# Performance work log

Hardware: AMD Instinct MI355X
Metric: run time of the kernel (lower is better)

## Reference

```python
import jax, jax.numpy as jnp
import numpy as np

EPS = 1e-12  # torch F.normalize eps


def setup_inputs() -> dict:
    key = jax.random.key(0)
    k1, k2, k3, k4, k5 = jax.random.split(key, 5)
    N, C, H, W = 32, 512, 32, 32
    E = 1024   # expansion * dim
    G = 8      # group
    D = E // G # 128, per-group channel dim
    K = 64     # num_clusters
    x = jax.random.normal(k1, (N, C, H, W), dtype=jnp.float32)
    W1 = jax.random.normal(k2, (E, C), dtype=jnp.float32) / np.sqrt(C)
    W2 = jax.random.normal(k3, (G, E), dtype=jnp.float32) / np.sqrt(E)
    Wc = jax.random.normal(k4, (K, D), dtype=jnp.float32) / np.sqrt(D)
    centroids = jax.random.uniform(k5, (K, D), dtype=jnp.float32)
    return {"x": x, "W1": W1, "W2": W2, "Wc": Wc, "centroids": centroids}


def reference(x, W1, W2, Wc, centroids):
    # x: [N, C, H, W]; W1: [E, C]; W2: [G, E]; Wc: [K, D]; centroids: [K, D]
    N, C, H, W = x.shape
    E = W1.shape[0]
    G = W2.shape[0]
    K, D = Wc.shape
    P = H * W
    # descriptor-wise L2 normalization over channel dim
    norm = jnp.linalg.norm(x, axis=1, keepdims=True)
    x = x / jnp.maximum(norm, EPS)
    # linear1 on channels: [N, E, P]
    xe = jnp.einsum('ncp,ec->nep', x.reshape(N, C, P), W1)
    # grouped features: [N, G, D, P]
    xg = xe.reshape(N, G, D, P)
    # attention gate: sigmoid(linear2)  -> [N, G, P]
    att = jax.nn.sigmoid(jnp.einsum('nep,ge->ngp', xe, W2))
    # 1x1 conv = per-pixel matmul with cluster weights -> [N, G, K, P]
    soft_assign = jax.nn.softmax(jnp.einsum('ngdp,kd->ngkp', xg, Wc), axis=2)
    # combined per-(cluster,pixel) weight
    w = soft_assign * att[:, :, None, :]  # [N, G, K, P]
    # NetVLAD residual aggregation, algebraically decomposed to avoid the
    # giant [N,G,K,D,P] intermediate:
    #   vlad[n,k,d] = sum_{g,p} w * xg  -  centroids[k,d] * sum_{g,p} w
    agg = jnp.einsum('ngkp,ngdp->nkd', w, xg)  # [N, K, D]
    wsum = w.sum(axis=(1, 3))                  # [N, K]
    vlad = agg - wsum[:, :, None] * centroids[None]  # [N, K, D]
    return vlad.reshape(N, K * D)
```

## Files before the change

kernel.cpp:

```cpp
#include <hip/hip_runtime.h>


#define N_  32
#define C_  512
#define P_  1024
#define E_  1024
#define G_  8
#define D_  128
#define K_  64

typedef __attribute__((ext_vector_type(8))) short bf16x8;
typedef __attribute__((ext_vector_type(4))) float f32x4;

__device__ __forceinline__ unsigned short f2b(float f) {
    union { float f; unsigned u; } v; v.f = f;
    unsigned r = (v.u + 0x7FFFu + ((v.u >> 16) & 1u)) >> 16;
    return (unsigned short)r;
}
__device__ __forceinline__ float b2f(unsigned short h) {
    union { unsigned u; float f; } v; v.u = ((unsigned)h) << 16;
    return v.f;
}

__device__ __forceinline__ void gl_lds16(const void* g, void* l) {
    __builtin_amdgcn_global_load_lds(
        (const __attribute__((address_space(1))) void*)g,
        (__attribute__((address_space(3))) void*)l, 16, 0, 0);
}

#define SB  __builtin_amdgcn_sched_barrier(0)
#define BAR __builtin_amdgcn_s_barrier()
#define WAITV(n_) asm volatile("s_waitcnt vmcnt(" #n_ ")" ::: "memory")

__global__ __launch_bounds__(256) void k0_prep(const float* __restrict__ W1,
                                               const float* __restrict__ Wc,
                                               const float* __restrict__ W2,
                                               unsigned short* __restrict__ W1b,
                                               unsigned short* __restrict__ Vb,
                                               unsigned short* __restrict__ Wa) {
    int bid = blockIdx.x;
    int t = threadIdx.x;
    if (bid < 1024) {
        int i0 = bid * 512 + t;
        W1b[i0]       = f2b(W1[i0]);
        W1b[i0 + 256] = f2b(W1[i0 + 256]);
        int ch = bid & 1, k = (bid >> 1) & 63, g = bid >> 7;
        int c = ch * 256 + t;
        float acc = 0.f;
        #pragma unroll 8
        for (int d = 0; d < 128; ++d)
            acc += Wc[k * 128 + d] * W1[(g * 128 + d) * C_ + c];
        Vb[(g * 64 + k) * C_ + c] = f2b(acc);
    } else {
        __shared__ float red[256];
        int idx = bid - 1024;
        int g  = idx >> 4;
        int c0 = (idx & 15) * 32;
        int c  = c0 + (t & 31);
        int ec = t >> 5;
        float acc = 0.f;
        #pragma unroll 8
        for (int i = 0; i < 128; ++i) {
            int e = ec * 128 + i;
            acc += W2[g * E_ + e] * W1[e * C_ + c];
        }
        red[t] = acc;
        __syncthreads();
        if (t < 32) {
            float s = 0.f;
            #pragma unroll
            for (int j = 0; j < 8; ++j) s += red[j * 32 + t];
            Wa[g * C_ + c0 + t] = f2b(s);
        }
    }
}

__global__ __launch_bounds__(256) void k1_norm_att(const float* __restrict__ x,
                                                   const unsigned short* __restrict__ Wa,
                                                   unsigned short* __restrict__ xhat_t,
                                                   float* __restrict__ att_s) {
    __shared__ short xc[128 * 256];
    __shared__ short waL[8 * 512];
    __shared__ float attP[2 * 64 * 8];
    __shared__ float red[256];
    int n = blockIdx.y;
    int p0 = blockIdx.x * 64;
    int t = threadIdx.x;
    int ps = t & 63, cs = t >> 6;

    #pragma unroll
    for (int i = 0; i < 2; ++i) {
        int ch = i * 256 + t;
        *(bf16x8*)&waL[ch * 8] = *(const bf16x8*)&Wa[ch * 8];
    }

    float ss = 0.f;
    for (int i = 0; i < 128; ++i) {
        float v = x[((size_t)(n * C_ + cs * 128 + i)) * P_ + p0 + ps];
        ss += v * v;
        xc[i * 256 + t] = (short)f2b(v);
    }
    red[t] = ss;
    __syncthreads();
    if (t < 64) {
        float s = red[t] + red[64 + t] + red[128 + t] + red[192 + t];
        red[t] = 1.0f / fmaxf(sqrtf(s), 1e-12f);
    }
    __syncthreads();

    float r = red[ps];
    float accA[8];
    #pragma unroll
    for (int g = 0; g < 8; ++g) accA[g] = 0.f;

    size_t base = ((size_t)(n * P_ + p0 + ps)) * C_ + cs * 128;
    #pragma unroll
    for (int jj = 0; jj < 16; ++jj) {
        bf16x8 o;
        float xv[8];
        #pragma unroll
        for (int j = 0; j < 8; ++j) {
            xv[j] = b2f((unsigned short)xc[(jj * 8 + j) * 256 + t]) * r;
            o[j] = (short)f2b(xv[j]);
        }
        *(bf16x8*)&xhat_t[base + jj * 8] = o;
        #pragma unroll
        for (int g = 0; g < 8; ++g) {
            bf16x8 wa = *(const bf16x8*)&waL[g * 512 + cs * 128 + jj * 8];
            #pragma unroll
            for (int j = 0; j < 8; ++j)
                accA[g] += b2f((unsigned short)wa[j]) * xv[j];
        }
    }

    if (cs & 1) {
        #pragma unroll
        for (int g = 0; g < 8; ++g)
            attP[((cs >> 1) * 64 + ps) * 8 + g] = accA[g];
    }
    __syncthreads();
    if (!(cs & 1)) {
        #pragma unroll
        for (int g = 0; g < 8; ++g)
            attP[((cs >> 1) * 64 + ps) * 8 + g] += accA[g];
    }
    __syncthreads();
    if (cs == 0) {
        #pragma unroll
        for (int g = 0; g < 8; ++g) {
            float s = attP[(0 * 64 + ps) * 8 + g] + attP[(1 * 64 + ps) * 8 + g];
            att_s[((size_t)(n * G_ + g)) * P_ + p0 + ps] = 1.0f / (1.0f + __expf(-s));
        }
    }
}

__global__ __launch_bounds__(256) void k2_gemm_xe(const unsigned short* __restrict__ W1b,
                                                  const unsigned short* __restrict__ xhat_t,
                                                  unsigned short* __restrict__ xe) {
    __shared__ __align__(16) short As[128 * 64];
    __shared__ __align__(16) short Bs[128 * 64];
    int n = blockIdx.y;
    int e0 = (blockIdx.x >> 3) * 128;
    int p0 = (blockIdx.x & 7) * 128;
    int t = threadIdx.x;
    int w = t >> 6, l = t & 63, q = l >> 4, l15 = l & 15;
    int wr = w >> 1, wc = w & 1;

    f32x4 acc[4][4];
    #pragma unroll
    for (int mi = 0; mi < 4; ++mi)
        #pragma unroll
        for (int ni = 0; ni < 4; ++ni)
            acc[mi][ni] = (f32x4){0.f, 0.f, 0.f, 0.f};

    for (int ks = 0; ks < 8; ++ks) {
        int k0 = ks * 64;
        #pragma unroll
        for (int i = 0; i < 4; ++i) {
            int ch = i * 256 + t;
            int row = ch >> 3, c8 = ch & 7;
            gl_lds16(&W1b[(e0 + row) * C_ + k0 + ((c8 ^ (row & 7)) * 8)], &As[ch * 8]);
        }
        #pragma unroll
        for (int i = 0; i < 4; ++i) {
            int ch = i * 256 + t;
            int row = ch >> 3, c8 = ch & 7;
            gl_lds16(&xhat_t[((size_t)(n * P_ + p0 + row)) * C_ + k0 + ((c8 ^ (row & 7)) * 8)], &Bs[ch * 8]);
        }
        __syncthreads();

        #pragma unroll
        for (int kk = 0; kk < 2; ++kk) {
            bf16x8 af[4], bf[4];
            #pragma unroll
            for (int mi = 0; mi < 4; ++mi)
                af[mi] = *(const bf16x8*)&As[(wr * 64 + mi * 16 + l15) * 64 + (((kk * 4 + q) ^ (l15 & 7)) * 8)];
            #pragma unroll
            for (int ni = 0; ni < 4; ++ni)
                bf[ni] = *(const bf16x8*)&Bs[(wc * 64 + ni * 16 + l15) * 64 + (((kk * 4 + q) ^ (l15 & 7)) * 8)];
            #pragma unroll
            for (int mi = 0; mi < 4; ++mi)
                #pragma unroll
                for (int ni = 0; ni < 4; ++ni)
                    acc[mi][ni] = __builtin_amdgcn_mfma_f32_16x16x32_bf16(af[mi], bf[ni], acc[mi][ni], 0, 0, 0);
        }
        __syncthreads();
    }

    #pragma unroll
    for (int mi = 0; mi < 4; ++mi) {
        #pragma unroll
        for (int ni = 0; ni < 4; ++ni) {
            #pragma unroll
            for (int r = 0; r < 4; ++r) {
                int e = e0 + wr * 64 + mi * 16 + q * 4 + r;
                int p = p0 + wc * 64 + ni * 16 + l15;
                xe[((size_t)(n * E_ + e)) * P_ + p] = f2b(acc[mi][ni][r]);
            }
        }
    }
}

__device__ __forceinline__ void stage_s(short* sb, const unsigned short* __restrict__ Vb,
                                        const unsigned short* __restrict__ xhat_t,
                                        int g, int n, int p0c, int k0, int t) {
    {
        int row = t >> 3, c8 = t & 7;
        gl_lds16(&Vb[(g * 64 + row) * C_ + k0 + ((c8 ^ (row & 7)) * 8)], &sb[t * 8]);
    }
    #pragma unroll
    for (int i = 0; i < 2; ++i) {
        int ch = i * 512 + t;
        int row = ch >> 3, c8 = ch & 7;
        gl_lds16(&xhat_t[((size_t)(n * P_ + p0c + row)) * C_ + k0 + ((c8 ^ (row & 7)) * 8)],
                 &sb[4096 + ch * 8]);
    }
}

__device__ __forceinline__ void stage_xg(short* xglds, const unsigned short* __restrict__ xe,
                                         int n, int g, int p0c, int t) {
    #pragma unroll
    for (int i = 0; i < 4; ++i) {
        int ch = i * 512 + t;
        int row = ch >> 4, c16 = ch & 15;
        gl_lds16(&xe[((size_t)(n * E_ + g * 128 + row)) * P_ + p0c + ((c16 ^ (row & 7)) * 8)],
                 &xglds[ch * 8]);
    }
}

__device__ __forceinline__ void mfma_s(f32x4 acc[4], const short* sb, int w, int q, int l15) {
    #pragma unroll
    for (int kk = 0; kk < 2; ++kk) {
        bf16x8 af[4], bfr;
        #pragma unroll
        for (int mi = 0; mi < 4; ++mi)
            af[mi] = *(const bf16x8*)&sb[(mi * 16 + l15) * 64 + (((kk * 4 + q) ^ (l15 & 7)) * 8)];
        bfr = *(const bf16x8*)&sb[4096 + (w * 16 + l15) * 64 + (((kk * 4 + q) ^ (l15 & 7)) * 8)];
        #pragma unroll
        for (int mi = 0; mi < 4; ++mi)
            acc[mi] = __builtin_amdgcn_mfma_f32_16x16x32_bf16(af[mi], bfr, acc[mi], 0, 0, 0);
    }
}

__global__ __launch_bounds__(512, 4) void k4_assign_agg(const unsigned short* __restrict__ Vb,
                                                        const unsigned short* __restrict__ xhat_t,
                                                        const unsigned short* __restrict__ xe,
                                                        const float* __restrict__ att_s,
                                                        float* __restrict__ agg_part,
                                                        float* __restrict__ wsum_part) {
    __shared__ __align__(16) char smem[81920];
    short* S0    = (short*)smem;
    short* S1    = (short*)(smem + 24576);
    short* xglds = (short*)(smem + 49152);
    short* wlds  = (short*)smem;
    float* wred  = (float*)smem;

    int b = blockIdx.y * 16 + blockIdx.x;
    int work = (b & 7) * 64 + (b >> 3);
    int n = work >> 4, g = work & 7, ph = (work >> 3) & 1;

    int t = threadIdx.x;
    int w = t >> 6, l = t & 63, q = l >> 4, l15 = l & 15;
    int kh = w >> 2, dq = w & 3;

    f32x4 acc_a[2][2];
    #pragma unroll
    for (int mi = 0; mi < 2; ++mi)
        #pragma unroll
        for (int ni = 0; ni < 2; ++ni)
            acc_a[mi][ni] = (f32x4){0.f, 0.f, 0.f, 0.f};
    float wsp[16];
    #pragma unroll
    for (int j = 0; j < 16; ++j) wsp[j] = 0.f;

#define RND(CUR, NXT, KN) \
    stage_s(NXT, Vb, xhat_t, g, n, p0c, (KN) * 64, t); \
    WAITV(3); BAR; SB; \
    mfma_s(acc_s, CUR, w, q, l15); \
    BAR; SB;

    #pragma unroll 1
    for (int cc = 0; cc < 4; ++cc) {
        int p0c = ph * 512 + cc * 128;

        float av = att_s[(((size_t)(n * G_ + g)) * P_) + p0c + w * 16 + l15];

        f32x4 acc_s[4];
        #pragma unroll
        for (int mi = 0; mi < 4; ++mi)
            acc_s[mi] = (f32x4){0.f, 0.f, 0.f, 0.f};

        stage_s(S0, Vb, xhat_t, g, n, p0c, 0, t);
        RND(S0, S1, 1)
        RND(S1, S0, 2)
        RND(S0, S1, 3)
        RND(S1, S0, 4)
        RND(S0, S1, 5)
        RND(S1, S0, 6)
        stage_s(S1, Vb, xhat_t, g, n, p0c, 448, t);
        stage_xg(xglds, xe, n, g, p0c, t);
        WAITV(7); BAR; SB;
        mfma_s(acc_s, S0, w, q, l15);
        BAR; SB;
        WAITV(4); BAR; SB;
        mfma_s(acc_s, S1, w, q, l15);
        BAR; SB;

        {
            float m = -1e30f;
            #pragma unroll
            for (int mi = 0; mi < 4; ++mi)
                #pragma unroll
                for (int r = 0; r < 4; ++r)
                    m = fmaxf(m, acc_s[mi][r]);
            m = fmaxf(m, __shfl_xor(m, 16));
            m = fmaxf(m, __shfl_xor(m, 32));
            float s = 0.f;
            #pragma unroll
            for (int mi = 0; mi < 4; ++mi)
                #pragma unroll
                for (int r = 0; r < 4; ++r) {
                    float e = __expf(acc_s[mi][r] - m);
                    acc_s[mi][r] = e;
                    s += e;
                }
            s += __shfl_xor(s, 16);
            s += __shfl_xor(s, 32);

            float scale = av / s;

            #pragma unroll
            for (int mi = 0; mi < 4; ++mi)
                #pragma unroll
                for (int r = 0; r < 4; ++r) {
                    float wv = acc_s[mi][r] * scale;
                    wsp[mi * 4 + r] += wv;
                    wlds[(mi * 16 + q * 4 + r) * 136 + (w * 16 + l15)] = (short)f2b(wv);
                }
        }
        __syncthreads();

        #pragma unroll
        for (int pk = 0; pk < 4; ++pk) {
            bf16x8 a2[2], b2[2];
            #pragma unroll
            for (int mi = 0; mi < 2; ++mi)
                a2[mi] = *(const bf16x8*)&wlds[(kh * 32 + mi * 16 + l15) * 136 + pk * 32 + q * 8];
            #pragma unroll
            for (int ni = 0; ni < 2; ++ni)
                b2[ni] = *(const bf16x8*)&xglds[(dq * 32 + ni * 16 + l15) * 128
                                                + (((pk * 4 + q) ^ (l15 & 7)) * 8)];
            #pragma unroll
            for (int mi = 0; mi < 2; ++mi)
                #pragma unroll
                for (int ni = 0; ni < 2; ++ni)
                    acc_a[mi][ni] = __builtin_amdgcn_mfma_f32_16x16x32_bf16(a2[mi], b2[ni], acc_a[mi][ni], 0, 0, 0);
        }
        __syncthreads();
    }

    size_t base = (((size_t)(n * G_ + g)) * 2 + ph) * 64;
    #pragma unroll
    for (int mi = 0; mi < 2; ++mi)
        #pragma unroll
        for (int ni = 0; ni < 2; ++ni)
            #pragma unroll
            for (int r = 0; r < 4; ++r) {
                int k = kh * 32 + mi * 16 + q * 4 + r;
                int d = dq * 32 + ni * 16 + l15;
                agg_part[(base + k) * 128 + d] = acc_a[mi][ni][r];
            }

    #pragma unroll
    for (int j = 0; j < 16; ++j) {
        float v = wsp[j];
        v += __shfl_xor(v, 1);
        v += __shfl_xor(v, 2);
        v += __shfl_xor(v, 4);
        v += __shfl_xor(v, 8);
        if (l15 == 0) {
            int k = (j >> 2) * 16 + q * 4 + (j & 3);
            wred[w * 64 + k] = v;
        }
    }
    __syncthreads();
    if (t < 64) {
        float s = 0.f;
        #pragma unroll
        for (int wv = 0; wv < 8; ++wv)
            s += wred[wv * 64 + t];
        wsum_part[(((size_t)(n * G_ + g)) * 2 + ph) * 64 + t] = s;
    }
}

__global__ __launch_bounds__(256) void k5_final(const float* __restrict__ agg_part,
                                                const float* __restrict__ wsum_part,
                                                const float* __restrict__ centroids,
                                                float* __restrict__ out) {
    int idx = blockIdx.x * 256 + threadIdx.x;
    int d = idx & 127;
    int k = (idx >> 7) & 63;
    int n = idx >> 13;
    float ws = 0.f;
    #pragma unroll
    for (int g = 0; g < 8; ++g)
        #pragma unroll
        for (int ph = 0; ph < 2; ++ph)
            ws += wsum_part[(((size_t)(n * G_ + g)) * 2 + ph) * 64 + k];
    float agg = 0.f;
    #pragma unroll
    for (int g = 0; g < 8; ++g)
        #pragma unroll
        for (int ph = 0; ph < 2; ++ph)
            agg += agg_part[(((((size_t)(n * G_ + g)) * 2 + ph) * 64) + k) * 128 + d];
    out[idx] = agg - ws * centroids[k * 128 + d];
}

extern "C" void kernel_launch(void* const* d_in, const int* in_sizes, int n_in,
                              void* d_out, int out_size, void* d_ws, size_t ws_size,
                              hipStream_t stream) {
    const float* x         = (const float*)d_in[0];
    const float* W1        = (const float*)d_in[1];
    const float* W2        = (const float*)d_in[2];
    const float* Wc        = (const float*)d_in[3];
    const float* centroids = (const float*)d_in[4];
    float* out = (float*)d_out;

    char* ws = (char*)d_ws;
    unsigned short* W1b      = (unsigned short*)(ws + 0);
    unsigned short* Vb       = (unsigned short*)(ws + 1048576);
    unsigned short* xhat_t   = (unsigned short*)(ws + 1572864);
    unsigned short* xe       = (unsigned short*)(ws + 35127296);
    float*          att_s    = (float*)(ws + 102236160);
    float*          agg_part = (float*)(ws + 103284736);
    float*          wsum_part= (float*)(ws + 120061952);
    unsigned short* Wa       = (unsigned short*)(ws + 120193024);

    hipLaunchKernelGGL(k0_prep,        dim3(1152), dim3(256), 0, stream, W1, Wc, W2, W1b, Vb, Wa);
    hipLaunchKernelGGL(k1_norm_att,    dim3(16, 32), dim3(256), 0, stream, x, Wa, xhat_t, att_s);
    hipLaunchKernelGGL(k2_gemm_xe,     dim3(64, 32), dim3(256), 0, stream, W1b, xhat_t, xe);
    hipLaunchKernelGGL(k4_assign_agg,  dim3(16, 32), dim3(512), 0, stream, Vb, xhat_t, xe,
                       att_s, agg_part, wsum_part);
    hipLaunchKernelGGL(k5_final,       dim3(1024), dim3(256), 0, stream,
                       agg_part, wsum_part, centroids, out);
}
```

Before: 212.3 us.

## Eliminate xe GEMM by reassociating aggregation through W1 in assign kernel

Drops the separate kernel that materialised xe = W1·xhat for every pixel and stops reading it back. The assign kernel now computes Y = w·xhat^T over the 512 input channels per group, staged from a new channel-major copy of xhat written by the norm kernel. It then multiplies Y by that group's W1 slice to form the aggregate. This removes a large bf16 intermediate write and read plus a full GEMM launch. In exchange the norm kernel does strided 2-byte scatter writes, the assign kernel holds many more accumulators (register pressure), and Y is rounded to bf16 before the second product.

```diff
diff --git a/kernel.cpp b/kernel.cpp
--- a/kernel.cpp
+++ b/kernel.cpp
@@ -78,6 +78,7 @@
 __global__ __launch_bounds__(256) void k1_norm_att(const float* __restrict__ x,
                                                    const unsigned short* __restrict__ Wa,
                                                    unsigned short* __restrict__ xhat_t,
+                                                   unsigned short* __restrict__ xhat_cp,
                                                    float* __restrict__ att_s) {
     __shared__ short xc[128 * 256];
     __shared__ short waL[8 * 512];
@@ -125,6 +126,11 @@
         }
         *(bf16x8*)&xhat_t[base + jj * 8] = o;
         #pragma unroll
+        for (int j = 0; j < 8; ++j) {
+            int c = cs * 128 + jj * 8 + j;
+            xhat_cp[((size_t)(n * C_ + c)) * P_ + p0 + ps] = (unsigned short)o[j];
+        }
+        #pragma unroll
         for (int g = 0; g < 8; ++g) {
             bf16x8 wa = *(const bf16x8*)&waL[g * 512 + cs * 128 + jj * 8];
             #pragma unroll
@@ -150,73 +156,6 @@
         for (int g = 0; g < 8; ++g) {
             float s = attP[(0 * 64 + ps) * 8 + g] + attP[(1 * 64 + ps) * 8 + g];
             att_s[((size_t)(n * G_ + g)) * P_ + p0 + ps] = 1.0f / (1.0f + __expf(-s));
-        }
-    }
-}
-
-__global__ __launch_bounds__(256) void k2_gemm_xe(const unsigned short* __restrict__ W1b,
-                                                  const unsigned short* __restrict__ xhat_t,
-                                                  unsigned short* __restrict__ xe) {
-    __shared__ __align__(16) short As[128 * 64];
-    __shared__ __align__(16) short Bs[128 * 64];
-    int n = blockIdx.y;
-    int e0 = (blockIdx.x >> 3) * 128;
-    int p0 = (blockIdx.x & 7) * 128;
-    int t = threadIdx.x;
-    int w = t >> 6, l = t & 63, q = l >> 4, l15 = l & 15;
-    int wr = w >> 1, wc = w & 1;
-
-    f32x4 acc[4][4];
-    #pragma unroll
-    for (int mi = 0; mi < 4; ++mi)
-        #pragma unroll
-        for (int ni = 0; ni < 4; ++ni)
-            acc[mi][ni] = (f32x4){0.f, 0.f, 0.f, 0.f};
-
-    for (int ks = 0; ks < 8; ++ks) {
-        int k0 = ks * 64;
-        #pragma unroll
-        for (int i = 0; i < 4; ++i) {
-            int ch = i * 256 + t;
-            int row = ch >> 3, c8 = ch & 7;
-            gl_lds16(&W1b[(e0 + row) * C_ + k0 + ((c8 ^ (row & 7)) * 8)], &As[ch * 8]);
-        }
-        #pragma unroll
-        for (int i = 0; i < 4; ++i) {
-            int ch = i * 256 + t;
-            int row = ch >> 3, c8 = ch & 7;
-            gl_lds16(&xhat_t[((size_t)(n * P_ + p0 + row)) * C_ + k0 + ((c8 ^ (row & 7)) * 8)], &Bs[ch * 8]);
-        }
-        __syncthreads();
-
-        #pragma unroll
-        for (int kk = 0; kk < 2; ++kk) {
-            bf16x8 af[4], bf[4];
-            #pragma unroll
-            for (int mi = 0; mi < 4; ++mi)
-                af[mi] = *(const bf16x8*)&As[(wr * 64 + mi * 16 + l15) * 64 + (((kk * 4 + q) ^ (l15 & 7)) * 8)];
-            #pragma unroll
-            for (int ni = 0; ni < 4; ++ni)
-                bf[ni] = *(const bf16x8*)&Bs[(wc * 64 + ni * 16 + l15) * 64 + (((kk * 4 + q) ^ (l15 & 7)) * 8)];
-            #pragma unroll
-            for (int mi = 0; mi < 4; ++mi)
-                #pragma unroll
-                for (int ni = 0; ni < 4; ++ni)
-                    acc[mi][ni] = __builtin_amdgcn_mfma_f32_16x16x32_bf16(af[mi], bf[ni], acc[mi][ni], 0, 0, 0);
-        }
-        __syncthreads();
-    }
-
-    #pragma unroll
-    for (int mi = 0; mi < 4; ++mi) {
-        #pragma unroll
-        for (int ni = 0; ni < 4; ++ni) {
-            #pragma unroll
-            for (int r = 0; r < 4; ++r) {
-                int e = e0 + wr * 64 + mi * 16 + q * 4 + r;
-                int p = p0 + wc * 64 + ni * 16 + l15;
-                xe[((size_t)(n * E_ + e)) * P_ + p] = f2b(acc[mi][ni][r]);
-            }
         }
     }
 }
@@ -237,14 +176,14 @@
     }
 }
 
-__device__ __forceinline__ void stage_xg(short* xglds, const unsigned short* __restrict__ xe,
-                                         int n, int g, int p0c, int t) {
-    #pragma unroll
-    for (int i = 0; i < 4; ++i) {
+__device__ __forceinline__ void stage_x(short* xb, const unsigned short* __restrict__ xhat_cp,
+                                        int n, int p0c, int c0, int t) {
+    #pragma unroll
+    for (int i = 0; i < 2; ++i) {
         int ch = i * 512 + t;
         int row = ch >> 4, c16 = ch & 15;
-        gl_lds16(&xe[((size_t)(n * E_ + g * 128 + row)) * P_ + p0c + ((c16 ^ (row & 7)) * 8)],
-                 &xglds[ch * 8]);
+        gl_lds16(&xhat_cp[((size_t)(n * C_ + c0 + row)) * P_ + p0c + ((c16 ^ (row & 7)) * 8)],
+                 &xb[ch * 8]);
     }
 }
 
@@ -262,18 +201,38 @@
     }
 }
 
+__device__ __forceinline__ void mfma_y(f32x4 Ysl[2], const short* wlds, const short* XB,
+                                       int kh, int dq, int q, int l15) {
+    #pragma unroll
+    for (int pk = 0; pk < 4; ++pk) {
+        bf16x8 a2[2], bx;
+        #pragma unroll
+        for (int mi = 0; mi < 2; ++mi)
+            a2[mi] = *(const bf16x8*)&wlds[(kh * 32 + mi * 16 + l15) * 136 + pk * 32 + q * 8];
+        bx = *(const bf16x8*)&XB[(dq * 16 + l15) * 128 + (((pk * 4 + q) ^ (l15 & 7)) * 8)];
+        #pragma unroll
+        for (int mi = 0; mi < 2; ++mi)
+            Ysl[mi] = __builtin_amdgcn_mfma_f32_16x16x32_bf16(a2[mi], bx, Ysl[mi], 0, 0, 0);
+    }
+}
+
 __global__ __launch_bounds__(512, 4) void k4_assign_agg(const unsigned short* __restrict__ Vb,
+                                                        const unsigned short* __restrict__ W1b,
                                                         const unsigned short* __restrict__ xhat_t,
-                                                        const unsigned short* __restrict__ xe,
+                                                        const unsigned short* __restrict__ xhat_cp,
                                                         const float* __restrict__ att_s,
                                                         float* __restrict__ agg_part,
                                                         float* __restrict__ wsum_part) {
     __shared__ __align__(16) char smem[81920];
-    short* S0    = (short*)smem;
-    short* S1    = (short*)(smem + 24576);
-    short* xglds = (short*)(smem + 49152);
-    short* wlds  = (short*)smem;
-    float* wred  = (float*)smem;
+    short* S0   = (short*)smem;
+    short* S1   = (short*)(smem + 24576);
+    short* X0   = (short*)smem;
+    short* X1   = (short*)(smem + 16384);
+    short* wlds = (short*)(smem + 49152);
+    short* Ylds = (short*)smem;
+    short* Wg   = (short*)(smem + 65536);
+    float* wred = (float*)smem;
+    float* wred2 = (float*)(smem + 65536);
 
     int b = blockIdx.y * 16 + blockIdx.x;
     int work = (b & 7) * 64 + (b >> 3);
@@ -283,12 +242,12 @@
     int w = t >> 6, l = t & 63, q = l >> 4, l15 = l & 15;
     int kh = w >> 2, dq = w & 3;
 
-    f32x4 acc_a[2][2];
-    #pragma unroll
-    for (int mi = 0; mi < 2; ++mi)
-        #pragma unroll
-        for (int ni = 0; ni < 2; ++ni)
-            acc_a[mi][ni] = (f32x4){0.f, 0.f, 0.f, 0.f};
+    f32x4 Y[8][2];
+    #pragma unroll
+    for (int sl = 0; sl < 8; ++sl)
+        #pragma unroll
+        for (int mi = 0; mi < 2; ++mi)
+            Y[sl][mi] = (f32x4){0.f, 0.f, 0.f, 0.f};
     float wsp[16];
     #pragma unroll
     for (int j = 0; j < 16; ++j) wsp[j] = 0.f;
@@ -297,6 +256,12 @@
     stage_s(NXT, Vb, xhat_t, g, n, p0c, (KN) * 64, t); \
     WAITV(3); BAR; SB; \
     mfma_s(acc_s, CUR, w, q, l15); \
+    BAR; SB;
+
+#define YRND(SL, CUR, NXT, CN) \
+    stage_x(NXT, xhat_cp, n, p0c, (CN) * 64, t); \
+    WAITV(2); BAR; SB; \
+    mfma_y(Y[SL], wlds, CUR, kh, dq, q, l15); \
     BAR; SB;
 
     #pragma unroll 1
@@ -317,12 +282,8 @@
         RND(S1, S0, 4)
         RND(S0, S1, 5)
         RND(S1, S0, 6)
-        stage_s(S1, Vb, xhat_t, g, n, p0c, 448, t);
-        stage_xg(xglds, xe, n, g, p0c, t);
-        WAITV(7); BAR; SB;
-        mfma_s(acc_s, S0, w, q, l15);
-        BAR; SB;
-        WAITV(4); BAR; SB;
+        RND(S0, S1, 7)
+        WAITV(0); BAR; SB;
         mfma_s(acc_s, S1, w, q, l15);
         BAR; SB;
 
@@ -360,23 +321,66 @@
         }
         __syncthreads();
 
-        #pragma unroll
-        for (int pk = 0; pk < 4; ++pk) {
-            bf16x8 a2[2], b2[2];
+        stage_x(X0, xhat_cp, n, p0c, 0, t);
+        YRND(0, X0, X1, 1)
+        YRND(1, X1, X0, 2)
+        YRND(2, X0, X1, 3)
+        YRND(3, X1, X0, 4)
+        YRND(4, X0, X1, 5)
+        YRND(5, X1, X0, 6)
+        YRND(6, X0, X1, 7)
+        WAITV(0); BAR; SB;
+        mfma_y(Y[7], wlds, X1, kh, dq, q, l15);
+        BAR; SB;
+    }
+
+    #pragma unroll
+    for (int sl = 0; sl < 8; ++sl)
+        #pragma unroll
+        for (int mi = 0; mi < 2; ++mi)
+            #pragma unroll
+            for (int r = 0; r < 4; ++r) {
+                int k = kh * 32 + mi * 16 + q * 4 + r;
+                int c = sl * 64 + dq * 16 + l15;
+                Ylds[k * 512 + (((c >> 3) ^ (k & 7)) * 8) + (c & 7)] = (short)f2b(Y[sl][mi][r]);
+            }
+    __syncthreads();
+
+    f32x4 acc_a[2][2];
+    #pragma unroll
+    for (int mi = 0; mi < 2; ++mi)
+        #pragma unroll
+        for (int ni = 0; ni < 2; ++ni)
+            acc_a[mi][ni] = (f32x4){0.f, 0.f, 0.f, 0.f};
+
+    #pragma unroll 1
+    for (int ks2 = 0; ks2 < 8; ++ks2) {
+        #pragma unroll
+        for (int i = 0; i < 2; ++i) {
+            int ch = i * 512 + t;
+            int row = ch >> 3, c8 = ch & 7;
+            gl_lds16(&W1b[((g * 128 + row) * C_) + ks2 * 64 + ((c8 ^ (row & 7)) * 8)],
+                     &Wg[ch * 8]);
+        }
+        WAITV(0); BAR; SB;
+        #pragma unroll
+        for (int kk = 0; kk < 2; ++kk) {
+            bf16x8 ay[2], bw[2];
             #pragma unroll
             for (int mi = 0; mi < 2; ++mi)
-                a2[mi] = *(const bf16x8*)&wlds[(kh * 32 + mi * 16 + l15) * 136 + pk * 32 + q * 8];
+                ay[mi] = *(const bf16x8*)&Ylds[(kh * 32 + mi * 16 + l15) * 512
+                                               + (((ks2 * 8 + kk * 4 + q) ^ (l15 & 7)) * 8)];
             #pragma unroll
             for (int ni = 0; ni < 2; ++ni)
-                b2[ni] = *(const bf16x8*)&xglds[(dq * 32 + ni * 16 + l15) * 128
-                                                + (((pk * 4 + q) ^ (l15 & 7)) * 8)];
+                bw[ni] = *(const bf16x8*)&Wg[(dq * 32 + ni * 16 + l15) * 64
+                                             + (((kk * 4 + q) ^ (l15 & 7)) * 8)];
             #pragma unroll
             for (int mi = 0; mi < 2; ++mi)
                 #pragma unroll
                 for (int ni = 0; ni < 2; ++ni)
-                    acc_a[mi][ni] = __builtin_amdgcn_mfma_f32_16x16x32_bf16(a2[mi], b2[ni], acc_a[mi][ni], 0, 0, 0);
-        }
-        __syncthreads();
+                    acc_a[mi][ni] = __builtin_amdgcn_mfma_f32_16x16x32_bf16(ay[mi], bw[ni], acc_a[mi][ni], 0, 0, 0);
+        }
+        BAR; SB;
     }
 
     size_t base = (((size_t)(n * G_ + g)) * 2 + ph) * 64;
@@ -400,7 +404,7 @@
         v += __shfl_xor(v, 8);
         if (l15 == 0) {
             int k = (j >> 2) * 16 + q * 4 + (j & 3);
-            wred[w * 64 + k] = v;
+            wred2[w * 64 + k] = v;
         }
     }
     __syncthreads();
@@ -408,9 +412,10 @@
         float s = 0.f;
         #pragma unroll
         for (int wv = 0; wv < 8; ++wv)
-            s += wred[wv * 64 + t];
+            s += wred2[wv * 64 + t];
         wsum_part[(((size_t)(n * G_ + g)) * 2 + ph) * 64 + t] = s;
     }
+    (void)wred;
 }
 
 __global__ __launch_bounds__(256) void k5_final(const float* __restrict__ agg_part,
@@ -450,17 +455,17 @@
     unsigned short* W1b      = (unsigned short*)(ws + 0);
     unsigned short* Vb       = (unsigned short*)(ws + 1048576);
     unsigned short* xhat_t   = (unsigned short*)(ws + 1572864);
-    unsigned short* xe       = (unsigned short*)(ws + 35127296);
+    unsigned short* xhat_cp  = (unsigned short*)(ws + 35127296);
     float*          att_s    = (float*)(ws + 102236160);
     float*          agg_part = (float*)(ws + 103284736);
     float*          wsum_part= (float*)(ws + 120061952);
     unsigned short* Wa       = (unsigned short*)(ws + 120193024);
 
     hipLaunchKernelGGL(k0_prep,        dim3(1152), dim3(256), 0, stream, W1, Wc, W2, W1b, Vb, Wa);
-    hipLaunchKernelGGL(k1_norm_att,    dim3(16, 32), dim3(256), 0, stream, x, Wa, xhat_t, att_s);
-    hipLaunchKernelGGL(k2_gemm_xe,     dim3(64, 32), dim3(256), 0, stream, W1b, xhat_t, xe);
-    hipLaunchKernelGGL(k4_assign_agg,  dim3(16, 32), dim3(512), 0, stream, Vb, xhat_t, xe,
-                       att_s, agg_part, wsum_part);
+    hipLaunchKernelGGL(k1_norm_att,    dim3(16, 32), dim3(256), 0, stream, x, Wa, xhat_t,
+                       xhat_cp, att_s);
+    hipLaunchKernelGGL(k4_assign_agg,  dim3(16, 32), dim3(512), 0, stream, Vb, W1b, xhat_t,
+                       xhat_cp, att_s, agg_part, wsum_part);
     hipLaunchKernelGGL(k5_final,       dim3(1024), dim3(256), 0, stream,
                        agg_part, wsum_part, centroids, out);
 }
```

After: 250.7 us. 18.1% more time.
